# Optimization experiments

Hardware: AMD Instinct MI355X
Metric: run time of the kernel (lower is better)

The kernel has to match this reference:

```python
import jax, jax.numpy as jnp
import numpy as np

B, N, F_IN, F_EMB = 2, 2048, 128, 64


def setup_inputs() -> dict:
    key = jax.random.key(0)
    k1, k2, k3 = jax.random.split(key, 3)
    x = jax.random.normal(k1, (B, N, F_IN), dtype=jnp.float32)
    # row-normalized random dense adjacency for the GCN-style embed_f
    A = jax.random.uniform(k2, (B, N, N), dtype=jnp.float32)
    A = A / jnp.sum(A, axis=-1, keepdims=True)
    W_embed = jax.random.normal(k3, (F_IN, F_EMB), dtype=jnp.float32) / np.sqrt(F_IN)
    b_embed = jnp.zeros((F_EMB,), dtype=jnp.float32)
    temperature = jnp.asarray(1.0, dtype=jnp.float32)   # nn.Parameter(tensor(1.))
    threshold = jnp.asarray(0.5, dtype=jnp.float32)     # nn.Parameter(tensor(0.5))
    return {"x": x, "A": A, "W_embed": W_embed, "b_embed": b_embed,
            "temperature": temperature, "threshold": threshold}


def reference(x, A, W_embed, b_embed, temperature, threshold):
    # embed_f: simple GCN-style layer relu(A @ x @ W + b)
    x_emb = jax.nn.relu(jnp.einsum('bnm,bmf->bnf', A, x) @ W_embed + b_embed)  # [B,N,E]

    # first-call centroid/scale (detached in torch -> stop_gradient)
    centroid = jax.lax.stop_gradient(jnp.mean(x_emb, axis=-2, keepdims=True))
    scale = jax.lax.stop_gradient(0.9 / jnp.max(jnp.abs(x_emb - centroid)))
    xs = (x_emb - centroid) * scale  # [B,N,E]

    # pairwise squared euclidean distances (cdist**2)
    sq = jnp.sum(xs * xs, axis=-1)  # [B,N]
    D = jnp.maximum(sq[:, :, None] + sq[:, None, :]
                    - 2.0 * jnp.einsum('bnd,bmd->bnm', xs, xs), 0.0)  # [B,N,N]

    adj = jax.nn.sigmoid(temperature * (jnp.abs(threshold) - D))  # strictly > 0

    # nonzero() on a strictly-positive sigmoid = ALL B*N*N entries, row-major,
    # with torch's batch offset: global_col = col + N * batch
    idx = jnp.arange(B * N * N, dtype=jnp.int64 if jax.config.x64_enabled else jnp.int32)
    rows = idx // N                      # flattened (batch*N + row) index
    cols = idx % N + N * (rows // N)     # col + N*batch offset
    edge_index = jnp.stack([rows, cols])  # [2, B*N*N]
    edges_weight = adj.reshape(-1)        # [B*N*N]

    return x_emb, edge_index, edges_weight
```

## Files before the change

### kernel.cpp

```cpp
#include <hip/hip_runtime.h>

#define NTOK 2048
#define BATCH 2
#define FIN 128
#define FEMB 64

typedef __attribute__((ext_vector_type(8))) short short8;
typedef __attribute__((ext_vector_type(4))) float floatx4;

#define MFMA_B16(a, b, c) __builtin_amdgcn_mfma_f32_16x16x32_bf16((a), (b), (c), 0, 0, 0)

static __device__ __forceinline__ unsigned short f2bf_bits(float f) {
    unsigned u = __float_as_uint(f);
    unsigned r = u + 0x7FFFu + ((u >> 16) & 1u);
    return (unsigned short)(r >> 16);
}
static __device__ __forceinline__ float bfbits2f(unsigned short h) {
    return __uint_as_float(((unsigned)h) << 16);
}

#define K1S 152
__global__ __launch_bounds__(256) void k_gemm_xwT(const float* __restrict__ x,
                                                  const float* __restrict__ W,
                                                  unsigned short* __restrict__ XwT) {
    __shared__ unsigned short As[64 * K1S];
    __shared__ unsigned short Bs[64 * K1S];
    int t = threadIdx.x;
    int n0 = blockIdx.x * 64;
#pragma unroll
    for (int c = 0; c < 32; ++c) {
        int idx = c * 256 + t;
        int k = idx >> 6, f = idx & 63;
        As[f * K1S + k] = f2bf_bits(W[idx]);
    }
#pragma unroll
    for (int c = 0; c < 4; ++c) {
        int e = c * 2048 + t * 8;
        int row = e >> 7, col = e & 127;
        const float* src = &x[(size_t)(n0 + row) * FIN + col];
        float4 f0 = *(const float4*)src;
        float4 f1 = *(const float4*)(src + 4);
        unsigned short h[8] = {f2bf_bits(f0.x), f2bf_bits(f0.y), f2bf_bits(f0.z),
                               f2bf_bits(f0.w), f2bf_bits(f1.x), f2bf_bits(f1.y),
                               f2bf_bits(f1.z), f2bf_bits(f1.w)};
        *(uint4*)&Bs[row * K1S + col] = *(uint4*)h;
    }
    __syncthreads();
    int w = t >> 6, l = t & 63, lm = l & 15, lq = l >> 4;
    floatx4 acc[4] = {};
#pragma unroll
    for (int kk = 0; kk < 128; kk += 32) {
        short8 a = *(const short8*)&As[(w * 16 + lm) * K1S + kk + lq * 8];
#pragma unroll
        for (int ct = 0; ct < 4; ++ct) {
            short8 b = *(const short8*)&Bs[(ct * 16 + lm) * K1S + kk + lq * 8];
            acc[ct] = MFMA_B16(a, b, acc[ct]);
        }
    }
#pragma unroll
    for (int ct = 0; ct < 4; ++ct)
#pragma unroll
        for (int r = 0; r < 4; ++r) {
            int f = w * 16 + lq * 4 + r;
            int tok = n0 + ct * 16 + lm;
            XwT[(size_t)f * (BATCH * NTOK) + tok] = f2bf_bits(acc[ct][r]);
        }
}

#define S2 280
__global__ __launch_bounds__(256) void k_gemm_xemb(const float* __restrict__ A,
                                                   const unsigned short* __restrict__ XwT,
                                                   const float* __restrict__ bvec,
                                                   float* __restrict__ xemb_out,
                                                   float* __restrict__ cent) {
    __shared__ unsigned short As[16 * S2];
    __shared__ unsigned short Bs[64 * S2];
    int t = threadIdx.x;
    int m0 = blockIdx.x * 16, b = blockIdx.y;
    const float* Ab = A + (size_t)b * NTOK * NTOK;
    int w = t >> 6, l = t & 63, lm = l & 15, lq = l >> 4;
    floatx4 acc = {};
    for (int k0 = 0; k0 < NTOK; k0 += 256) {
        __syncthreads();
        {
            int row = t >> 4, colb = (t & 15) * 16;
            const float* src = &Ab[(size_t)(m0 + row) * NTOK + k0 + colb];
            unsigned short h[16];
#pragma unroll
            for (int i = 0; i < 4; ++i) {
                float4 v = *(const float4*)(src + i * 4);
                h[i * 4 + 0] = f2bf_bits(v.x);
                h[i * 4 + 1] = f2bf_bits(v.y);
                h[i * 4 + 2] = f2bf_bits(v.z);
                h[i * 4 + 3] = f2bf_bits(v.w);
            }
            *(uint4*)&As[row * S2 + colb] = *(uint4*)&h[0];
            *(uint4*)&As[row * S2 + colb + 8] = *(uint4*)&h[8];
            int f = t >> 2, cb = (t & 3) * 64;
            const unsigned short* bs = &XwT[(size_t)f * (BATCH * NTOK) + b * NTOK + k0 + cb];
#pragma unroll
            for (int i = 0; i < 8; ++i)
                *(uint4*)&Bs[f * S2 + cb + i * 8] = *(const uint4*)(bs + i * 8);
        }
        __syncthreads();
#pragma unroll
        for (int kk = 0; kk < 256; kk += 32) {
            short8 a = *(const short8*)&As[lm * S2 + kk + lq * 8];
            short8 bb = *(const short8*)&Bs[(w * 16 + lm) * S2 + kk + lq * 8];
            acc = MFMA_B16(a, bb, acc);
        }
    }
    int f = w * 16 + lm;
    float bias = bvec[f];
    float s = 0.f;
#pragma unroll
    for (int r = 0; r < 4; ++r) {
        int m = m0 + lq * 4 + r;
        float v = fmaxf(acc[r] + bias, 0.0f);
        xemb_out[(size_t)b * NTOK * FEMB + (size_t)m * FEMB + f] = v;
        s += v;
    }
    s += __shfl_xor(s, 16, 64);
    s += __shfl_xor(s, 32, 64);
    if (lq == 0) atomicAdd(&cent[b * 64 + f], s);
}

__global__ void k_maxabs(const float* __restrict__ xemb, const float* __restrict__ cent,
                         unsigned* __restrict__ mx) {
    int gid = blockIdx.x * 256 + threadIdx.x;
    int i4 = gid * 4;
    int b = i4 >> 17, f = i4 & 63;
    float4 v = *(const float4*)&xemb[i4];
    float4 c = *(const float4*)&cent[b * 64 + f];
    float m = fmaxf(fmaxf(fabsf(v.x - c.x * (1.0f / NTOK)), fabsf(v.y - c.y * (1.0f / NTOK))),
                    fmaxf(fabsf(v.z - c.z * (1.0f / NTOK)), fabsf(v.w - c.w * (1.0f / NTOK))));
#pragma unroll
    for (int off = 32; off; off >>= 1) m = fmaxf(m, __shfl_xor(m, off, 64));
    if ((threadIdx.x & 63) == 0) atomicMax(mx, __float_as_uint(m));
}

__global__ void k_xs_sq(const float* __restrict__ xemb, const float* __restrict__ cent,
                        const unsigned* __restrict__ mx,
                        unsigned short* __restrict__ xs, float* __restrict__ sq) {
    int t = threadIdx.x;
    int row = blockIdx.x * 4 + (t >> 6);
    int f = t & 63;
    int b = row >> 11;
    float scale = 0.9f / __uint_as_float(*mx);
    float c = cent[b * 64 + f] * (1.0f / NTOK);
    float v = (xemb[(size_t)row * FEMB + f] - c) * scale;
    unsigned short hb = f2bf_bits(v);
    xs[(size_t)row * FEMB + f] = hb;
    float d = bfbits2f(hb);
    float s = d * d;
#pragma unroll
    for (int off = 32; off; off >>= 1) s += __shfl_xor(s, off, 64);
    if (f == 0) sq[row] = s;
}

#define K5S 88
__global__ __launch_bounds__(256) void k_adj_edges(const unsigned short* __restrict__ xs,
                                                   const float* __restrict__ sq,
                                                   const float* __restrict__ temp,
                                                   const float* __restrict__ thr,
                                                   float* __restrict__ wout,
                                                   float* __restrict__ eout) {
    int z = blockIdx.z;
    if (z >= 2) {
        int eb = (z - 2) * 256 + blockIdx.y * 16 + blockIdx.x;
        long base0 = (long)eb * 32768 + threadIdx.x * 4;
#pragma unroll
        for (int j = 0; j < 32; ++j) {
            long g = base0 + (long)j * 1024;
            float4 v;
            if (g < 8388608L) {
                float r = (float)(g >> 11);
                v.x = r; v.y = r; v.z = r; v.w = r;
            } else {
                long rel = g - 8388608L;
                int c0 = (int)(rel & 2047);
                int add = ((int)(rel >> 22)) << 11;
                v.x = (float)(c0 + 0 + add);
                v.y = (float)(c0 + 1 + add);
                v.z = (float)(c0 + 2 + add);
                v.w = (float)(c0 + 3 + add);
            }
            *(float4*)&eout[g] = v;
        }
        return;
    }
    __shared__ unsigned short As[128 * K5S];
    __shared__ unsigned short Bs[128 * K5S];
    int t = threadIdx.x;
    int m0 = blockIdx.x * 128, n0 = blockIdx.y * 128, b = z;
    const unsigned short* xb = xs + (size_t)b * NTOK * FEMB;
#pragma unroll
    for (int c = 0; c < 4; ++c) {
        int e = c * 2048 + t * 8;
        int row = e >> 6, col = e & 63;
        *(uint4*)&As[row * K5S + col] = *(const uint4*)&xb[(size_t)(m0 + row) * FEMB + col];
        *(uint4*)&Bs[row * K5S + col] = *(const uint4*)&xb[(size_t)(n0 + row) * FEMB + col];
    }
    __syncthreads();
    int w = t >> 6, l = t & 63, lm = l & 15, lq = l >> 4;
    floatx4 acc[2][8] = {};
#pragma unroll
    for (int kk = 0; kk < 64; kk += 32) {
        short8 a0 = *(const short8*)&As[((w * 2 + 0) * 16 + lm) * K5S + kk + lq * 8];
        short8 a1 = *(const short8*)&As[((w * 2 + 1) * 16 + lm) * K5S + kk + lq * 8];
#pragma unroll
        for (int ct = 0; ct < 8; ++ct) {
            short8 bb = *(const short8*)&Bs[(ct * 16 + lm) * K5S + kk + lq * 8];
            acc[0][ct] = MFMA_B16(a0, bb, acc[0][ct]);
            acc[1][ct] = MFMA_B16(a1, bb, acc[1][ct]);
        }
    }
    float tval = temp[0];
    float ath = fabsf(thr[0]);
    float sqm[2][4], sqn[8];
#pragma unroll
    for (int rt = 0; rt < 2; ++rt)
#pragma unroll
        for (int r = 0; r < 4; ++r)
            sqm[rt][r] = sq[b * NTOK + m0 + (w * 2 + rt) * 16 + lq * 4 + r];
#pragma unroll
    for (int ct = 0; ct < 8; ++ct) sqn[ct] = sq[b * NTOK + n0 + ct * 16 + lm];
    float* wob = wout + (size_t)b * NTOK * NTOK;
#pragma unroll
    for (int rt = 0; rt < 2; ++rt)
#pragma unroll
        for (int r = 0; r < 4; ++r) {
            int m = m0 + (w * 2 + rt) * 16 + lq * 4 + r;
#pragma unroll
            for (int ct = 0; ct < 8; ++ct) {
                float g = acc[rt][ct][r];
                float D = fmaxf(sqm[rt][r] + sqn[ct] - 2.0f * g, 0.0f);
                float z2 = tval * (ath - D);
                float wgt = 1.0f / (1.0f + __expf(-z2));
                wob[(size_t)m * NTOK + n0 + ct * 16 + lm] = wgt;
            }
        }
}

extern "C" void kernel_launch(void* const* d_in, const int* in_sizes, int n_in,
                              void* d_out, int out_size, void* d_ws, size_t ws_size,
                              hipStream_t stream) {
    const float* x    = (const float*)d_in[0];
    const float* A    = (const float*)d_in[1];
    const float* W    = (const float*)d_in[2];
    const float* bvec = (const float*)d_in[3];
    const float* temp = (const float*)d_in[4];
    const float* thr  = (const float*)d_in[5];
    float* out = (float*)d_out;
    char* ws = (char*)d_ws;

    unsigned short* XwT = (unsigned short*)(ws + 0);
    float*          cent= (float*)(ws + 524288);
    unsigned*       mx  = (unsigned*)(ws + 524800);
    unsigned short* xs  = (unsigned short*)(ws + 524816);
    float*          sq  = (float*)(ws + 1049104);

    float* xemb_out = out;
    float* edge_out = out + 262144;
    float* wgt_out  = out + 262144 + 16777216;

    hipMemsetAsync(ws + 524288, 0, 520, stream);

    k_gemm_xwT<<<64, 256, 0, stream>>>(x, W, XwT);
    k_gemm_xemb<<<dim3(128, 2), 256, 0, stream>>>(A, XwT, bvec, xemb_out, cent);
    k_maxabs<<<256, 256, 0, stream>>>(xemb_out, cent, mx);
    k_xs_sq<<<1024, 256, 0, stream>>>(xemb_out, cent, mx, xs, sq);
    k_adj_edges<<<dim3(16, 16, 4), 256, 0, stream>>>(xs, sq, temp, thr, wgt_out, edge_out);
}
```

Baseline: 176.0 us.

## Drop centering kernel by computing distances from raw embeddings with scale squared

Pairwise squared distances do not change when every point is shifted by the same centroid. The adjacency kernel now works on uncentered bf16 embeddings and their squared norms, and multiplies the result by scale squared. This removes the separate centering/normalisation kernel and the memset, since the accumulators are zeroed inside the first GEMM. The A@XW GEMM is rewritten as a split-K over 8 waves that read global memory directly and reduce through LDS, and the XW GEMM uses smaller tiles across more blocks. The risk is bf16 cancellation: raw embeddings have larger norms than centered ones, so D may lose accuracy.

```diff
diff --git a/kernel.cpp b/kernel.cpp
--- a/kernel.cpp
+++ b/kernel.cpp
@@ -22,11 +22,13 @@
 #define K1S 152
 __global__ __launch_bounds__(256) void k_gemm_xwT(const float* __restrict__ x,
                                                   const float* __restrict__ W,
-                                                  unsigned short* __restrict__ XwT) {
+                                                  unsigned short* __restrict__ XwT,
+                                                  unsigned* __restrict__ centmx) {
     __shared__ unsigned short As[64 * K1S];
-    __shared__ unsigned short Bs[64 * K1S];
+    __shared__ unsigned short Bs[32 * K1S];
     int t = threadIdx.x;
-    int n0 = blockIdx.x * 64;
+    int n0 = blockIdx.x * 32;
+    if (blockIdx.x == 0 && t < 129) centmx[t] = 0;
 #pragma unroll
     for (int c = 0; c < 32; ++c) {
         int idx = c * 256 + t;
@@ -34,7 +36,7 @@
         As[f * K1S + k] = f2bf_bits(W[idx]);
     }
 #pragma unroll
-    for (int c = 0; c < 4; ++c) {
+    for (int c = 0; c < 2; ++c) {
         int e = c * 2048 + t * 8;
         int row = e >> 7, col = e & 127;
         const float* src = &x[(size_t)(n0 + row) * FIN + col];
@@ -47,18 +49,18 @@
     }
     __syncthreads();
     int w = t >> 6, l = t & 63, lm = l & 15, lq = l >> 4;
-    floatx4 acc[4] = {};
+    floatx4 acc[2] = {};
 #pragma unroll
     for (int kk = 0; kk < 128; kk += 32) {
         short8 a = *(const short8*)&As[(w * 16 + lm) * K1S + kk + lq * 8];
 #pragma unroll
-        for (int ct = 0; ct < 4; ++ct) {
+        for (int ct = 0; ct < 2; ++ct) {
             short8 b = *(const short8*)&Bs[(ct * 16 + lm) * K1S + kk + lq * 8];
             acc[ct] = MFMA_B16(a, b, acc[ct]);
         }
     }
 #pragma unroll
-    for (int ct = 0; ct < 4; ++ct)
+    for (int ct = 0; ct < 2; ++ct)
 #pragma unroll
         for (int r = 0; r < 4; ++r) {
             int f = w * 16 + lq * 4 + r;
@@ -67,62 +69,70 @@
         }
 }
 
-#define S2 280
-__global__ __launch_bounds__(256) void k_gemm_xemb(const float* __restrict__ A,
+#define RP 66
+__global__ __launch_bounds__(512) void k_gemm_xemb(const float* __restrict__ A,
                                                    const unsigned short* __restrict__ XwT,
                                                    const float* __restrict__ bvec,
                                                    float* __restrict__ xemb_out,
+                                                   unsigned short* __restrict__ xebf,
+                                                   float* __restrict__ q,
                                                    float* __restrict__ cent) {
-    __shared__ unsigned short As[16 * S2];
-    __shared__ unsigned short Bs[64 * S2];
+    __shared__ float red[8][16][RP];
     int t = threadIdx.x;
     int m0 = blockIdx.x * 16, b = blockIdx.y;
-    const float* Ab = A + (size_t)b * NTOK * NTOK;
     int w = t >> 6, l = t & 63, lm = l & 15, lq = l >> 4;
-    floatx4 acc = {};
-    for (int k0 = 0; k0 < NTOK; k0 += 256) {
-        __syncthreads();
-        {
-            int row = t >> 4, colb = (t & 15) * 16;
-            const float* src = &Ab[(size_t)(m0 + row) * NTOK + k0 + colb];
-            unsigned short h[16];
-#pragma unroll
-            for (int i = 0; i < 4; ++i) {
-                float4 v = *(const float4*)(src + i * 4);
-                h[i * 4 + 0] = f2bf_bits(v.x);
-                h[i * 4 + 1] = f2bf_bits(v.y);
-                h[i * 4 + 2] = f2bf_bits(v.z);
-                h[i * 4 + 3] = f2bf_bits(v.w);
-            }
-            *(uint4*)&As[row * S2 + colb] = *(uint4*)&h[0];
-            *(uint4*)&As[row * S2 + colb + 8] = *(uint4*)&h[8];
-            int f = t >> 2, cb = (t & 3) * 64;
-            const unsigned short* bs = &XwT[(size_t)f * (BATCH * NTOK) + b * NTOK + k0 + cb];
-#pragma unroll
-            for (int i = 0; i < 8; ++i)
-                *(uint4*)&Bs[f * S2 + cb + i * 8] = *(const uint4*)(bs + i * 8);
-        }
-        __syncthreads();
-#pragma unroll
-        for (int kk = 0; kk < 256; kk += 32) {
-            short8 a = *(const short8*)&As[lm * S2 + kk + lq * 8];
-            short8 bb = *(const short8*)&Bs[(w * 16 + lm) * S2 + kk + lq * 8];
-            acc = MFMA_B16(a, bb, acc);
-        }
-    }
-    int f = w * 16 + lm;
-    float bias = bvec[f];
-    float s = 0.f;
-#pragma unroll
-    for (int r = 0; r < 4; ++r) {
-        int m = m0 + lq * 4 + r;
-        float v = fmaxf(acc[r] + bias, 0.0f);
-        xemb_out[(size_t)b * NTOK * FEMB + (size_t)m * FEMB + f] = v;
-        s += v;
-    }
-    s += __shfl_xor(s, 16, 64);
-    s += __shfl_xor(s, 32, 64);
-    if (lq == 0) atomicAdd(&cent[b * 64 + f], s);
+    const float* Arow =
+        A + (size_t)b * NTOK * NTOK + (size_t)(m0 + lm) * NTOK + w * 256 + lq * 8;
+    const unsigned short* Bbase = XwT + b * NTOK + w * 256 + lq * 8;
+    floatx4 acc[4] = {};
+#pragma unroll
+    for (int kk = 0; kk < 256; kk += 32) {
+        float4 a0 = *(const float4*)(Arow + kk);
+        float4 a1 = *(const float4*)(Arow + kk + 4);
+        unsigned short h[8] = {f2bf_bits(a0.x), f2bf_bits(a0.y), f2bf_bits(a0.z),
+                               f2bf_bits(a0.w), f2bf_bits(a1.x), f2bf_bits(a1.y),
+                               f2bf_bits(a1.z), f2bf_bits(a1.w)};
+        short8 af = *(short8*)h;
+#pragma unroll
+        for (int ct = 0; ct < 4; ++ct) {
+            short8 bf = *(const short8*)(Bbase + (size_t)(ct * 16 + lm) * (BATCH * NTOK) + kk);
+            acc[ct] = MFMA_B16(af, bf, acc[ct]);
+        }
+    }
+#pragma unroll
+    for (int ct = 0; ct < 4; ++ct)
+#pragma unroll
+        for (int r = 0; r < 4; ++r)
+            red[w][lq * 4 + r][ct * 16 + lm] = acc[ct][r];
+    __syncthreads();
+    int r = t >> 5, c0 = (t & 31) * 2;
+    float v0 = 0.f, v1 = 0.f;
+#pragma unroll
+    for (int ww = 0; ww < 8; ++ww) {
+        v0 += red[ww][r][c0];
+        v1 += red[ww][r][c0 + 1];
+    }
+    v0 = fmaxf(v0 + bvec[c0], 0.0f);
+    v1 = fmaxf(v1 + bvec[c0 + 1], 0.0f);
+    size_t o = (size_t)b * NTOK * FEMB + (size_t)(m0 + r) * FEMB + c0;
+    *(float2*)&xemb_out[o] = make_float2(v0, v1);
+    unsigned short h0 = f2bf_bits(v0), h1 = f2bf_bits(v1);
+    *(unsigned*)&xebf[o] = (unsigned)h0 | ((unsigned)h1 << 16);
+    float d0 = bfbits2f(h0), d1 = bfbits2f(h1);
+    float s = d0 * d0 + d1 * d1;
+#pragma unroll
+    for (int off = 16; off; off >>= 1) s += __shfl_xor(s, off, 64);
+    if ((t & 31) == 0) q[b * NTOK + m0 + r] = s;
+    __syncthreads();
+    red[0][r][c0] = v0;
+    red[0][r][c0 + 1] = v1;
+    __syncthreads();
+    if (t < 64) {
+        float cs = 0.f;
+#pragma unroll
+        for (int rr = 0; rr < 16; ++rr) cs += red[0][rr][t];
+        atomicAdd(&cent[b * 64 + t], cs);
+    }
 }
 
 __global__ void k_maxabs(const float* __restrict__ xemb, const float* __restrict__ cent,
@@ -139,28 +149,10 @@
     if ((threadIdx.x & 63) == 0) atomicMax(mx, __float_as_uint(m));
 }
 
-__global__ void k_xs_sq(const float* __restrict__ xemb, const float* __restrict__ cent,
-                        const unsigned* __restrict__ mx,
-                        unsigned short* __restrict__ xs, float* __restrict__ sq) {
-    int t = threadIdx.x;
-    int row = blockIdx.x * 4 + (t >> 6);
-    int f = t & 63;
-    int b = row >> 11;
-    float scale = 0.9f / __uint_as_float(*mx);
-    float c = cent[b * 64 + f] * (1.0f / NTOK);
-    float v = (xemb[(size_t)row * FEMB + f] - c) * scale;
-    unsigned short hb = f2bf_bits(v);
-    xs[(size_t)row * FEMB + f] = hb;
-    float d = bfbits2f(hb);
-    float s = d * d;
-#pragma unroll
-    for (int off = 32; off; off >>= 1) s += __shfl_xor(s, off, 64);
-    if (f == 0) sq[row] = s;
-}
-
 #define K5S 88
-__global__ __launch_bounds__(256) void k_adj_edges(const unsigned short* __restrict__ xs,
-                                                   const float* __restrict__ sq,
+__global__ __launch_bounds__(256) void k_adj_edges(const unsigned short* __restrict__ xebf,
+                                                   const float* __restrict__ q,
+                                                   const unsigned* __restrict__ mx,
                                                    const float* __restrict__ temp,
                                                    const float* __restrict__ thr,
                                                    float* __restrict__ wout,
@@ -174,8 +166,8 @@
             long g = base0 + (long)j * 1024;
             float4 v;
             if (g < 8388608L) {
-                float r = (float)(g >> 11);
-                v.x = r; v.y = r; v.z = r; v.w = r;
+                float rr = (float)(g >> 11);
+                v.x = rr; v.y = rr; v.z = rr; v.w = rr;
             } else {
                 long rel = g - 8388608L;
                 int c0 = (int)(rel & 2047);
@@ -193,7 +185,7 @@
     __shared__ unsigned short Bs[128 * K5S];
     int t = threadIdx.x;
     int m0 = blockIdx.x * 128, n0 = blockIdx.y * 128, b = z;
-    const unsigned short* xb = xs + (size_t)b * NTOK * FEMB;
+    const unsigned short* xb = xebf + (size_t)b * NTOK * FEMB;
 #pragma unroll
     for (int c = 0; c < 4; ++c) {
         int e = c * 2048 + t * 8;
@@ -215,16 +207,18 @@
             acc[1][ct] = MFMA_B16(a1, bb, acc[1][ct]);
         }
     }
+    float sc = 0.9f / __uint_as_float(*mx);
+    float s2 = sc * sc;
     float tval = temp[0];
     float ath = fabsf(thr[0]);
-    float sqm[2][4], sqn[8];
+    float qm[2][4], qn[8];
 #pragma unroll
     for (int rt = 0; rt < 2; ++rt)
 #pragma unroll
         for (int r = 0; r < 4; ++r)
-            sqm[rt][r] = sq[b * NTOK + m0 + (w * 2 + rt) * 16 + lq * 4 + r];
-#pragma unroll
-    for (int ct = 0; ct < 8; ++ct) sqn[ct] = sq[b * NTOK + n0 + ct * 16 + lm];
+            qm[rt][r] = q[b * NTOK + m0 + (w * 2 + rt) * 16 + lq * 4 + r];
+#pragma unroll
+    for (int ct = 0; ct < 8; ++ct) qn[ct] = q[b * NTOK + n0 + ct * 16 + lm];
     float* wob = wout + (size_t)b * NTOK * NTOK;
 #pragma unroll
     for (int rt = 0; rt < 2; ++rt)
@@ -234,7 +228,7 @@
 #pragma unroll
             for (int ct = 0; ct < 8; ++ct) {
                 float g = acc[rt][ct][r];
-                float D = fmaxf(sqm[rt][r] + sqn[ct] - 2.0f * g, 0.0f);
+                float D = s2 * fmaxf(qm[rt][r] + qn[ct] - 2.0f * g, 0.0f);
                 float z2 = tval * (ath - D);
                 float wgt = 1.0f / (1.0f + __expf(-z2));
                 wob[(size_t)m * NTOK + n0 + ct * 16 + lm] = wgt;
@@ -254,21 +248,19 @@
     float* out = (float*)d_out;
     char* ws = (char*)d_ws;
 
-    unsigned short* XwT = (unsigned short*)(ws + 0);
-    float*          cent= (float*)(ws + 524288);
-    unsigned*       mx  = (unsigned*)(ws + 524800);
-    unsigned short* xs  = (unsigned short*)(ws + 524816);
-    float*          sq  = (float*)(ws + 1049104);
+    unsigned short* XwT  = (unsigned short*)(ws + 0);
+    float*          cent = (float*)(ws + 524288);
+    unsigned*       mx   = (unsigned*)(ws + 524800);
+    unsigned short* xebf = (unsigned short*)(ws + 524816);
+    float*          q    = (float*)(ws + 1049104);
 
     float* xemb_out = out;
     float* edge_out = out + 262144;
     float* wgt_out  = out + 262144 + 16777216;
 
-    hipMemsetAsync(ws + 524288, 0, 520, stream);
-
-    k_gemm_xwT<<<64, 256, 0, stream>>>(x, W, XwT);
-    k_gemm_xemb<<<dim3(128, 2), 256, 0, stream>>>(A, XwT, bvec, xemb_out, cent);
+    k_gemm_xwT<<<128, 256, 0, stream>>>(x, W, XwT, (unsigned*)(ws + 524288));
+    k_gemm_xemb<<<dim3(128, 2), 512, 0, stream>>>(A, XwT, bvec, xemb_out, xebf, q, cent);
     k_maxabs<<<256, 256, 0, stream>>>(xemb_out, cent, mx);
-    k_xs_sq<<<1024, 256, 0, stream>>>(xemb_out, cent, mx, xs, sq);
-    k_adj_edges<<<dim3(16, 16, 4), 256, 0, stream>>>(xs, sq, temp, thr, wgt_out, edge_out);
-}
+    k_adj_edges<<<dim3(16, 16, 4), 256, 0, stream>>>(xebf, q, mx, temp, thr,
+                                                     wgt_out, edge_out);
+}
```

New measurement: 169.5 us. 1.04x faster.
